# Kernel optimization log

Hardware: AMD Instinct MI355X
Metric: run time of the kernel (lower is better)

Reference implementation:

```python
import jax, jax.numpy as jnp
import numpy as np

B, S, H = 2, 4096, 2048          # batch, seq_len, hidden_size
NH, D, W = 8, 128, 4             # num_kv_heads, head_dim, conv_kernel_size (window)
KD = NH * D                      # key_dim == value_dim == 1024
ROPE_BASE = 1000000.0
EPS = 1e-6


def _rope_tables(d, end, base):
    inv = 1.0 / (base ** (np.arange(0, d, 2)[: d // 2].astype(np.float32) / d))
    f = np.outer(np.arange(end, dtype=np.float32), inv)  # [end, d/2]
    return jnp.asarray(np.cos(f)), jnp.asarray(np.sin(f))


def _apply_rope(x, cos, sin):
    # x: [B,S,h,d]; llama-style interleaved pairs (2i, 2i+1)
    x0, x1 = x[..., 0::2], x[..., 1::2]
    c = cos[None, :, None, :]
    s = sin[None, :, None, :]
    o0 = x0 * c - x1 * s
    o1 = x0 * s + x1 * c
    return jnp.stack([o0, o1], axis=-1).reshape(x.shape)


def setup_inputs() -> dict:
    key = jax.random.key(0)
    ks = jax.random.split(key, 7)
    sd = lambda k, shape, fan_in: jax.random.normal(k, shape, jnp.float32) * (fan_in ** -0.5)
    return {
        "x": jax.random.normal(ks[0], (B, S, H), jnp.float32),
        "W_qkv": sd(ks[1], (H, 3 * KD), H),
        "W_z": sd(ks[2], (H, KD), H),
        "W_b": sd(ks[3], (H, NH), H),
        "W_a": sd(ks[4], (H, NH), H),
        "norm_w": jnp.ones((KD,), jnp.float32),
        "W_out": sd(ks[5], (KD, H), KD),
    }


def _forward(x, W_qkv, W_z, W_b, W_a, norm_w, W_out):
    cos, sin = _rope_tables(D, S, ROPE_BASE)
    qkv = x @ W_qkv
    q, k, v = qkv[..., :KD], qkv[..., KD:2 * KD], qkv[..., 2 * KD:]
    z = x @ W_z           # [B,S,KD]
    bg = x @ W_b          # [B,S,NH]
    ag = x @ W_a          # [B,S,NH]

    q4 = _apply_rope(q.reshape(B, S, NH, D), cos, sin)
    k4 = _apply_rope(k.reshape(B, S, NH, D), cos, sin)
    v4 = v.reshape(B, S, NH, D)

    # Windowed gated delta rule: out[i] = sum_{j=i-W..i} (q_i.k_j/sqrt(D)) * sigmoid(a_i*b_j) * v_j
    # Implemented per diagonal offset (W+1 small, fixed) -- never materializes an SxS matrix.
    scale = 1.0 / np.sqrt(D).astype(np.float32)
    out = jnp.zeros_like(v4)
    idx = jnp.arange(S)
    for off in range(W + 1):
        if off == 0:
            kj, vj, bj = k4, v4, bg
        else:
            kj = jnp.pad(k4, ((0, 0), (off, 0), (0, 0), (0, 0)))[:, :S]
            vj = jnp.pad(v4, ((0, 0), (off, 0), (0, 0), (0, 0)))[:, :S]
            bj = jnp.pad(bg, ((0, 0), (off, 0), (0, 0)))[:, :S]
        score = jnp.einsum('bshd,bshd->bsh', q4, kj) * scale
        s = score * jax.nn.sigmoid(ag * bj)
        s = jnp.where((idx >= off)[None, :, None], s, 0.0)
        out = out + s[..., None] * vj
    # position 0 bypasses the attention entirely: output[0] = v[0]
    out = out.at[:, 0].set(v4[:, 0])

    y = out.reshape(B, S, KD) * jax.nn.sigmoid(z)
    # GatedRMSNorm(y, z): rmsnorm(y) * weight * silu(z)
    yf = y.reshape(B * S, KD)
    zf = z.reshape(B * S, KD)
    rms = jnp.sqrt(jnp.mean(yf * yf, axis=-1, keepdims=True) + EPS)
    yn = (yf / rms) * norm_w * (zf * jax.nn.sigmoid(zf))
    return yn.reshape(B, S, KD) @ W_out


def reference(x, W_qkv, W_z, W_b, W_a, norm_w, W_out):
    return _forward(x, W_qkv, W_z, W_b, W_a, norm_w, W_out)
```

## Files before the change

### kernel.cpp

```cpp
#include <hip/hip_runtime.h>
#include <hip/hip_bf16.h>
#include <stdint.h>

#define B_   2
#define S_   4096
#define H_   2048
#define NH_  8
#define D_   128
#define KD_  1024
#define MR   (B_ * S_)
#define NQKVZ 4096

typedef __attribute__((ext_vector_type(8))) short bf16x8;
typedef __attribute__((ext_vector_type(4))) float f32x4;

__device__ __forceinline__ short f2bf(float f) {
    union { float f; uint32_t u; } v; v.f = f;
    uint32_t r = v.u + 0x7FFF + ((v.u >> 16) & 1);
    return (short)(r >> 16);
}
__device__ __forceinline__ float bf2f(unsigned short u) {
    union { uint32_t u; float f; } v; v.u = (uint32_t)u << 16; return v.f;
}

__device__ __forceinline__ void async_ld16(const void* g, void* l) {
    __builtin_amdgcn_global_load_lds(
        (const __attribute__((address_space(1))) uint32_t*)g,
        (__attribute__((address_space(3))) uint32_t*)l, 16, 0, 0);
}

__global__ __launch_bounds__(256) void k_cvt_bgag(const float* __restrict__ x,
                                                  short* __restrict__ xb,
                                                  const float* __restrict__ Wb,
                                                  const float* __restrict__ Wa,
                                                  float* __restrict__ bgag) {
    const int m = blockIdx.x, t = threadIdx.x;
    __shared__ float xs[2048];
    __shared__ float part[256];
    const float4* xr = (const float4*)(x + (size_t)m * H_);
    float4 a = xr[t], b = xr[t + 256];
    ((float4*)xs)[t] = a;
    ((float4*)xs)[t + 256] = b;
    short4 oa, ob;
    oa.x = f2bf(a.x); oa.y = f2bf(a.y); oa.z = f2bf(a.z); oa.w = f2bf(a.w);
    ob.x = f2bf(b.x); ob.y = f2bf(b.y); ob.z = f2bf(b.z); ob.w = f2bf(b.w);
    short4* xo = (short4*)(xb + (size_t)m * H_);
    xo[t] = oa;
    xo[t + 256] = ob;
    __syncthreads();
    int col = t & 15, seg = t >> 4;
    const float* W = (col < 8) ? Wb : Wa;
    int c = col & 7;
    float acc = 0.f;
    int kb = seg * 128;
    for (int k = 0; k < 128; k++) acc += xs[kb + k] * W[(size_t)(kb + k) * 8 + c];
    part[t] = acc;
    __syncthreads();
    if (t < 16) {
        float s = 0.f;
        for (int j = 0; j < 16; j++) s += part[j * 16 + t];
        bgag[(size_t)m * 16 + t] = s;
    }
}

__global__ __launch_bounds__(256) void k_transpose_cvt(const float* __restrict__ W,
                                                       short* __restrict__ Wt,
                                                       int K, int N) {
    __shared__ float tile[32][33];
    int n0 = blockIdx.x * 32, k0 = blockIdx.y * 32;
    int tx = threadIdx.x, ty = threadIdx.y;
#pragma unroll
    for (int i = 0; i < 32; i += 8)
        tile[ty + i][tx] = W[(size_t)(k0 + ty + i) * N + n0 + tx];
    __syncthreads();
#pragma unroll
    for (int i = 0; i < 32; i += 8)
        Wt[(size_t)(n0 + ty + i) * K + k0 + tx] = f2bf(tile[tx][ty + i]);
}

__global__ __launch_bounds__(256) void k_ropetab(float2* __restrict__ ctab) {
    int idx = blockIdx.x * 256 + threadIdx.x;
    int i = idx & 63, s = idx >> 6;
    float inv = exp2f(-(float)i * (2.0f / 128.0f) * 19.931568569324174f);
    float f = (float)s * inv;
    float sn, cs;
    sincosf(f, &sn, &cs);
    ctab[idx] = make_float2(cs, sn);
}

#define PHASE_TAIL() \
    __builtin_amdgcn_s_setprio(0); \
    asm volatile("s_waitcnt vmcnt(%0)" :: "n"(2 * (2 + LB)) : "memory"); \
    asm volatile("s_waitcnt lgkmcnt(0)" ::: "memory"); \
    asm volatile("s_barrier" ::: "memory")
#define LDA_ALL(KH) \
    _Pragma("unroll") for (int i = 0; i < 8; i++) \
        afr[i] = *(const bf16x8*)(base + (KH) * AHB + (wm + i * 16 + mrow) * 64 + kcA)
#define LDB_F(KH) \
    _Pragma("unroll") for (int j = 0; j < NF; j++) \
        bfr[j] = *(const bf16x8*)(base + 2 * AHB + (KH) * BHB + (wn + j * 16 + mrow) * 64 + kcA)
#define MFMA_ALL() \
    _Pragma("unroll") for (int i = 0; i < 8; i++) \
    _Pragma("unroll") for (int j = 0; j < NF; j++) \
        acc[i][j] = __builtin_amdgcn_mfma_f32_16x16x32_bf16(afr[i], bfr[j], acc[i][j], 0, 0, 0)

template <int BN, int EPI>
__global__ __launch_bounds__(512, 2) void k_gemm256(const short* __restrict__ A,
                                                    const short* __restrict__ Bt,
                                                    float* __restrict__ Cf,
                                                    unsigned short* __restrict__ Cb,
                                                    const float2* __restrict__ ctab,
                                                    int M, int N, int K) {
    constexpr int BM = 256;
    constexpr int NF = BN / 64;
    constexpr int LB = BN / 128;
    constexpr int AHB = BM * 64;
    constexpr int BHB = BN * 64;
    constexpr int BUFB = 2 * AHB + 2 * BHB;
    __shared__ __align__(16) char lds[2 * BUFB];

    const int t = threadIdx.x;
    const int lane = t & 63, wave = t >> 6;
    const int mrow = lane & 15;
    const int kcA = (((lane >> 4) ^ ((mrow >> 1) & 3)) * 16);

    const int nwg = gridDim.x;
    const int w0 = blockIdx.x;
    const int wg = (w0 & 7) * (nwg >> 3) + (w0 >> 3);
    const int NB = N / BN;
    const int bn = (wg % NB) * BN;
    const int bm = (wg / NB) * BM;

    const int wm = (wave >> 2) * 128;
    const int wn = (wave & 3) * (BN / 4);

    const short* __restrict__ Ab = A + (size_t)bm * K;
    const short* __restrict__ Bb = Bt + (size_t)bn * K;

    int aoff[2], adst[2];
#pragma unroll
    for (int l = 0; l < 2; l++) {
        int c = t + l * 512;
        int row = c >> 2;
        int kcg = (c & 3) ^ ((row >> 1) & 3);
        aoff[l] = row * K + kcg * 8;
        adst[l] = c * 16;
    }
    int boff[LB], bdst[LB];
#pragma unroll
    for (int l = 0; l < LB; l++) {
        int c = t + l * 512;
        int row = c >> 2;
        int kcg = (c & 3) ^ ((row >> 1) & 3);
        boff[l] = row * K + kcg * 8;
        bdst[l] = c * 16;
    }

    const int NT = K >> 6;

    auto stageA = [&](int kt, int kh, int p) {
        const short* g = Ab + kt * 64 + kh * 32;
        char* d = lds + p * BUFB + kh * AHB;
#pragma unroll
        for (int l = 0; l < 2; l++) async_ld16(g + aoff[l], d + adst[l]);
    };
    auto stageB = [&](int kt, int kh, int p) {
        const short* g = Bb + kt * 64 + kh * 32;
        char* d = lds + p * BUFB + 2 * AHB + kh * BHB;
#pragma unroll
        for (int l = 0; l < LB; l++) async_ld16(g + boff[l], d + bdst[l]);
    };

    f32x4 acc[8][NF] = {};

    stageA(0, 0, 0); stageB(0, 0, 0);
    stageA(0, 1, 0); stageB(0, 1, 0);
    {
        int k1 = (NT > 1) ? 1 : 0;
        stageA(k1, 0, 1); stageB(k1, 0, 1);
    }
    asm volatile("s_waitcnt vmcnt(%0)" :: "n"(2 * (2 + LB)) : "memory");
    asm volatile("s_barrier" ::: "memory");

    for (int kt = 0; kt < NT; kt++) {
        const int p = kt & 1;
        const char* base = lds + p * BUFB;
        const int k1 = (kt + 1 < NT) ? (kt + 1) : (NT - 1);
        const int k2 = (kt + 2 < NT) ? (kt + 2) : (NT - 1);
        bf16x8 afr[8], bfr[NF];

        LDB_F(0);
        LDA_ALL(0);
        stageA(k1, 1, p ^ 1); stageB(k1, 1, p ^ 1);
        __builtin_amdgcn_s_setprio(1);
        MFMA_ALL();
        PHASE_TAIL();

        LDB_F(1);
        LDA_ALL(1);
        stageA(k2, 0, p); stageB(k2, 0, p);
        __builtin_amdgcn_s_setprio(1);
        MFMA_ALL();
        PHASE_TAIL();
    }
    asm volatile("s_waitcnt vmcnt(0)" ::: "memory");

    const int crow = (lane >> 4) * 4, ccol = lane & 15;
#pragma unroll
    for (int i = 0; i < 8; i++)
#pragma unroll
        for (int j = 0; j < NF; j++) {
            const int col = bn + wn + j * 16 + ccol;
            const int rowb = bm + wm + i * 16 + crow;
            size_t basec = (size_t)rowb * N + col;
            if (EPI == 0) {
#pragma unroll
                for (int r = 0; r < 4; r++)
                    Cf[basec + (size_t)r * N] = acc[i][j][r];
            } else {
                const bool qk = col < 2048;
                const int fi = (col & 127) >> 1;
                const bool even = (col & 1) == 0;
                uint32_t* Cd = (uint32_t*)(Cb + ((size_t)rowb * N + (col & ~1)));
#pragma unroll
                for (int r = 0; r < 4; r++) {
                    float v = acc[i][j][r];
                    if (qk) {
                        int s = (rowb + r) & (S_ - 1);
                        float2 cs = ctab[s * 64 + fi];
                        float pp = __shfl_xor(v, 1);
                        v = even ? v * cs.x - pp * cs.y : v * cs.x + pp * cs.y;
                    }
                    int hb = (int)(unsigned short)f2bf(v);
                    int pb = __shfl_xor(hb, 1);
                    if (even)
                        Cd[(size_t)r * (N >> 1)] = (uint32_t)(hb | (pb << 16));
                }
            }
        }
}

__global__ __launch_bounds__(256) void k_attn(const unsigned short* __restrict__ qkvz,
                                              const float* __restrict__ bgag,
                                              const float* __restrict__ norm_w,
                                              short* __restrict__ yn) {
    const int m = blockIdx.x;
    const int s = m & (S_ - 1);
    const int t = threadIdx.x;
    __shared__ unsigned short kvls[5][2048];
    __shared__ unsigned short qzls[2048];
    __shared__ float sc[NH_][5];
    __shared__ float red[4];
    const int nOff = (s < 4 ? s : 4) + 1;

    for (int off = 0; off < 5; off++) {
        if (off < nOff) {
            const ushort4* r = (const ushort4*)(qkvz + (size_t)(m - off) * NQKVZ + 1024);
            ushort4* d = (ushort4*)kvls[off];
            d[t] = r[t];
            d[t + 256] = r[t + 256];
        }
    }
    {
        const unsigned short* r = qkvz + (size_t)m * NQKVZ;
        ushort4* d = (ushort4*)qzls;
        d[t] = ((const ushort4*)r)[t];
        d[256 + t] = ((const ushort4*)(r + 3072))[t];
    }
    __syncthreads();

    {
        const int h = t >> 5, l = t & 31;
        float qv[4];
#pragma unroll
        for (int d = 0; d < 4; d++) qv[d] = bf2f(qzls[h * 128 + l * 4 + d]);
        const float ag = bgag[(size_t)m * 16 + 8 + h];
#pragma unroll
        for (int off = 0; off < 5; off++) {
            float acc = 0.f;
            if (off < nOff) {
#pragma unroll
                for (int d = 0; d < 4; d++)
                    acc += qv[d] * bf2f(kvls[off][h * 128 + l * 4 + d]);
            }
#pragma unroll
            for (int w = 1; w < 32; w <<= 1) acc += __shfl_xor(acc, w);
            if (l == 0) {
                float val = 0.f;
                if (off < nOff) {
                    float bg = bgag[(size_t)(m - off) * 16 + h];
                    float g = 1.f / (1.f + expf(-ag * bg));
                    val = acc * 0.08838834764831845f * g;
                }
                sc[h][off] = val;
            }
        }
    }
    __syncthreads();

    const int e0 = t * 4, h = e0 >> 7;
    float o[4] = {0.f, 0.f, 0.f, 0.f};
    if (s == 0) {
#pragma unroll
        for (int d = 0; d < 4; d++) o[d] = bf2f(kvls[0][1024 + e0 + d]);
    } else {
        for (int off = 0; off < nOff; off++) {
            float w = sc[h][off];
#pragma unroll
            for (int d = 0; d < 4; d++) o[d] += w * bf2f(kvls[off][1024 + e0 + d]);
        }
    }
    float y[4], zs4[4], ss = 0.f;
#pragma unroll
    for (int d = 0; d < 4; d++) {
        float z = bf2f(qzls[1024 + e0 + d]);
        float sg = 1.f / (1.f + expf(-z));
        y[d] = o[d] * sg;
        zs4[d] = z * sg;
        ss += y[d] * y[d];
    }
    const int wave = t >> 6, lane = t & 63;
#pragma unroll
    for (int w = 1; w < 64; w <<= 1) ss += __shfl_xor(ss, w);
    if (lane == 0) red[wave] = ss;
    __syncthreads();
    float tot = red[0] + red[1] + red[2] + red[3];
    float rinv = 1.f / sqrtf(tot * (1.0f / 1024.0f) + 1e-6f);
    short4 ov;
    ov.x = f2bf(y[0] * rinv * norm_w[e0 + 0] * zs4[0]);
    ov.y = f2bf(y[1] * rinv * norm_w[e0 + 1] * zs4[1]);
    ov.z = f2bf(y[2] * rinv * norm_w[e0 + 2] * zs4[2]);
    ov.w = f2bf(y[3] * rinv * norm_w[e0 + 3] * zs4[3]);
    ((short4*)yn)[(size_t)m * 256 + t] = ov;
}

extern "C" void kernel_launch(void* const* d_in, const int* in_sizes, int n_in,
                              void* d_out, int out_size, void* d_ws, size_t ws_size,
                              hipStream_t stream) {
    const float* x      = (const float*)d_in[0];
    const float* W_qkv  = (const float*)d_in[1];
    const float* W_z    = (const float*)d_in[2];
    const float* W_b    = (const float*)d_in[3];
    const float* W_a    = (const float*)d_in[4];
    const float* norm_w = (const float*)d_in[5];
    const float* W_out  = (const float*)d_in[6];
    float* out = (float*)d_out;

    char* ws = (char*)d_ws;
    short* xb    = (short*)ws;          ws += (size_t)MR * H_ * 2;
    short* Wt1   = (short*)ws;          ws += (size_t)NQKVZ * H_ * 2;
    short* Wt2   = (short*)ws;          ws += (size_t)H_ * KD_ * 2;
    unsigned short* qkvzb = (unsigned short*)ws; ws += (size_t)MR * NQKVZ * 2;
    float* bgag  = (float*)ws;          ws += (size_t)MR * 16 * 4;
    short* yn    = (short*)ws;          ws += (size_t)MR * KD_ * 2;
    float2* ctab = (float2*)ws;         ws += (size_t)S_ * 64 * 8;

    k_cvt_bgag<<<MR, 256, 0, stream>>>(x, xb, W_b, W_a, bgag);
    k_transpose_cvt<<<dim3(3072 / 32, 2048 / 32), dim3(32, 8), 0, stream>>>(W_qkv, Wt1, 2048, 3072);
    k_transpose_cvt<<<dim3(1024 / 32, 2048 / 32), dim3(32, 8), 0, stream>>>(W_z, Wt1 + (size_t)3072 * 2048, 2048, 1024);
    k_transpose_cvt<<<dim3(2048 / 32, 1024 / 32), dim3(32, 8), 0, stream>>>(W_out, Wt2, 1024, 2048);
    k_ropetab<<<S_ * 64 / 256, 256, 0, stream>>>(ctab);
    k_gemm256<256, 1><<<(MR / 256) * (NQKVZ / 256), 512, 0, stream>>>(
        xb, Wt1, nullptr, qkvzb, ctab, MR, NQKVZ, H_);
    k_attn<<<MR, 256, 0, stream>>>(qkvzb, bgag, norm_w, yn);
    k_gemm256<256, 0><<<(MR / 256) * (H_ / 256), 512, 0, stream>>>(
        yn, Wt2, out, nullptr, nullptr, MR, H_, KD_);
}
```

Before: 471.4 us.

## Software-pipeline LDS fragment loads one half-step ahead of MFMA in GEMM

Restructures the GEMM main loop so the A/B fragments for the next k-half are read from LDS while the current half's MFMAs run, using even/odd register sets plus a staging set for rows 4-7. The explicit lgkmcnt(0) wait is dropped and the vmcnt threshold is tightened to match the changed pipeline depth, with sched_barrier used to fix instruction order. The aim is to hide LDS read latency behind matrix math. In exchange it raises register pressure under 2-waves-per-SIMD launch bounds and makes the correctness of the LDS hazard ordering depend on the barrier and wait placement.

```diff
diff --git a/kernel.cpp b/kernel.cpp
--- a/kernel.cpp
+++ b/kernel.cpp
@@ -90,19 +90,24 @@
 
 #define PHASE_TAIL() \
     __builtin_amdgcn_s_setprio(0); \
-    asm volatile("s_waitcnt vmcnt(%0)" :: "n"(2 * (2 + LB)) : "memory"); \
-    asm volatile("s_waitcnt lgkmcnt(0)" ::: "memory"); \
+    asm volatile("s_waitcnt vmcnt(%0)" :: "n"(2 + LB) : "memory"); \
     asm volatile("s_barrier" ::: "memory")
-#define LDA_ALL(KH) \
-    _Pragma("unroll") for (int i = 0; i < 8; i++) \
-        afr[i] = *(const bf16x8*)(base + (KH) * AHB + (wm + i * 16 + mrow) * 64 + kcA)
-#define LDB_F(KH) \
+#define LDB_P(SET, BASE, KH) \
     _Pragma("unroll") for (int j = 0; j < NF; j++) \
-        bfr[j] = *(const bf16x8*)(base + 2 * AHB + (KH) * BHB + (wn + j * 16 + mrow) * 64 + kcA)
-#define MFMA_ALL() \
-    _Pragma("unroll") for (int i = 0; i < 8; i++) \
+        bf##SET[j] = *(const bf16x8*)((BASE) + 2 * AHB + (KH) * BHB + (wn + j * 16 + mrow) * 64 + kcA)
+#define LDA03_P(SET, BASE, KH) \
+    _Pragma("unroll") for (int i = 0; i < 4; i++) \
+        af##SET[i] = *(const bf16x8*)((BASE) + (KH) * AHB + (wm + i * 16 + mrow) * 64 + kcA)
+#define LDA47_S(BASE, KH) \
+    _Pragma("unroll") for (int i = 0; i < 4; i++) \
+        afS[i] = *(const bf16x8*)((BASE) + (KH) * AHB + (wm + 64 + i * 16 + mrow) * 64 + kcA)
+#define MFMA_PH(SET) \
+    _Pragma("unroll") for (int i = 0; i < 4; i++) \
     _Pragma("unroll") for (int j = 0; j < NF; j++) \
-        acc[i][j] = __builtin_amdgcn_mfma_f32_16x16x32_bf16(afr[i], bfr[j], acc[i][j], 0, 0, 0)
+        acc[i][j] = __builtin_amdgcn_mfma_f32_16x16x32_bf16(af##SET[i], bf##SET[j], acc[i][j], 0, 0, 0); \
+    _Pragma("unroll") for (int i = 0; i < 4; i++) \
+    _Pragma("unroll") for (int j = 0; j < NF; j++) \
+        acc[4 + i][j] = __builtin_amdgcn_mfma_f32_16x16x32_bf16(afS[i], bf##SET[j], acc[4 + i][j], 0, 0, 0)
 
 template <int BN, int EPI>
 __global__ __launch_bounds__(512, 2) void k_gemm256(const short* __restrict__ A,
@@ -172,6 +177,7 @@
     };
 
     f32x4 acc[8][NF] = {};
+    bf16x8 afE[4], bfE[NF], afO[4], bfO[NF], afS[4];
 
     stageA(0, 0, 0); stageB(0, 0, 0);
     stageA(0, 1, 0); stageB(0, 1, 0);
@@ -181,26 +187,31 @@
     }
     asm volatile("s_waitcnt vmcnt(%0)" :: "n"(2 * (2 + LB)) : "memory");
     asm volatile("s_barrier" ::: "memory");
+    LDB_P(E, lds, 0); LDA03_P(E, lds, 0);
+    asm volatile("s_waitcnt vmcnt(%0)" :: "n"(2 + LB) : "memory");
+    asm volatile("s_barrier" ::: "memory");
 
     for (int kt = 0; kt < NT; kt++) {
         const int p = kt & 1;
         const char* base = lds + p * BUFB;
+        const char* baseN = lds + (p ^ 1) * BUFB;
         const int k1 = (kt + 1 < NT) ? (kt + 1) : (NT - 1);
         const int k2 = (kt + 2 < NT) ? (kt + 2) : (NT - 1);
-        bf16x8 afr[8], bfr[NF];
-
-        LDB_F(0);
-        LDA_ALL(0);
+
+        LDA47_S(base, 0);
+        LDB_P(O, base, 1); LDA03_P(O, base, 1);
         stageA(k1, 1, p ^ 1); stageB(k1, 1, p ^ 1);
+        __builtin_amdgcn_sched_barrier(0);
         __builtin_amdgcn_s_setprio(1);
-        MFMA_ALL();
+        MFMA_PH(E);
         PHASE_TAIL();
 
-        LDB_F(1);
-        LDA_ALL(1);
+        LDA47_S(base, 1);
+        LDB_P(E, baseN, 0); LDA03_P(E, baseN, 0);
         stageA(k2, 0, p); stageB(k2, 0, p);
+        __builtin_amdgcn_sched_barrier(0);
         __builtin_amdgcn_s_setprio(1);
-        MFMA_ALL();
+        MFMA_PH(O);
         PHASE_TAIL();
     }
     asm volatile("s_waitcnt vmcnt(0)" ::: "memory");
```

Result: no change. 471.0 us (-0.1%).
